# Optimization experiments

Measured on AMD Instinct MI355X. Metric: run time of the kernel, lower is better.

## Reference

```python
import jax, jax.numpy as jnp
import numpy as np

NUM_BINS = 8
TAIL_BOUND = 3.0
MIN_V = 1e-3
MIN_DERIV = 1e-3


def _normalize(u):
    # softmax -> min-width floor -> cumsum -> pad left -> map to [-tail, tail]
    v = jax.nn.softmax(u, axis=-1)
    v = MIN_V + (1.0 - MIN_V * NUM_BINS) * v
    cum = jnp.cumsum(v, axis=-1)
    cum = jnp.pad(cum, [(0, 0)] * (cum.ndim - 1) + [(1, 0)])
    return (cum - 0.5) * 2.0 * TAIL_BOUND, v


def _rqs(x_dyn, u_w, u_h, u_d):
    # x_dyn: [B, D]; u_w/u_h: [B, D, K]; u_d: [B, D, K+1]
    cum_w, w = _normalize(u_w)
    cum_h, h = _normalize(u_h)
    d = jax.nn.softplus(u_d) + MIN_DERIV
    cum_w = cum_w.at[..., -1].add(1e-6)  # searchsorted eps on last edge

    idx = jnp.sum((x_dyn[..., None] >= cum_w).astype(jnp.int32), axis=-1) - 1
    idx = jnp.clip(idx, 0, NUM_BINS - 1)[..., None]  # [B, D, 1]

    take = lambda a, i: jnp.take_along_axis(a, i, axis=-1)[..., 0]
    cw, ww = take(cum_w, idx), take(w, idx)
    ch, hh = take(cum_h, idx), take(h, idx)
    di = jnp.clip(take(d, idx), MIN_DERIV, 1000.0)
    di1 = jnp.clip(take(d, idx + 1), MIN_DERIV, 1000.0)

    delta = hh / ww
    theta = jnp.clip((x_dyn - cw) / ww, 0.0, 1.0)
    t1m = theta * (1.0 - theta)
    num_term = di1 * theta ** 2 + delta * t1m
    den = jnp.maximum(delta + (di + di1 - 2.0 * delta) * t1m, 1e-6)
    spline_out = ch + delta * num_term / den * ww
    deriv_num = delta ** 2 * (di1 * theta ** 2 + 2.0 * delta * t1m + di * (1.0 - theta) ** 2)
    spline_logdet = jnp.log(jnp.maximum(deriv_num / den ** 2, 1e-12))

    in_range = (x_dyn >= -TAIL_BOUND) & (x_dyn <= TAIL_BOUND)
    out = jnp.where(in_range, spline_out, x_dyn)
    logdet = jnp.where(in_range, spline_logdet, 0.0)
    return out, logdet


def setup_inputs() -> dict:
    key = jax.random.key(0)
    ks = jax.random.split(key, 3)
    B, D, H = 32768, 128, 256
    total = 3 * NUM_BINS + 1
    x = jax.random.normal(ks[0], (B, D), dtype=jnp.float32)
    mask = (jnp.arange(D) % 2).astype(jnp.float32)
    W1 = jax.random.normal(ks[1], (D, H), dtype=jnp.float32) * (1.0 / np.sqrt(D))
    b1 = jnp.zeros((H,), dtype=jnp.float32)
    W2 = jax.random.normal(ks[2], (H, D * total), dtype=jnp.float32) * (1.0 / np.sqrt(H))
    b2 = jnp.zeros((D * total,), dtype=jnp.float32)
    return {"x": x, "mask": mask, "W1": W1, "b1": b1, "W2": W2, "b2": b2}


def reference(x, mask, W1, b1, W2, b2):
    B, D = x.shape
    total = 3 * NUM_BINS + 1
    x_static = x * mask
    x_dyn = x * (1.0 - mask)
    hidden = jax.nn.relu(x_static @ W1 + b1)
    params = (hidden @ W2 + b2).reshape(B, D, total)
    u_w = params[..., :NUM_BINS]
    u_h = params[..., NUM_BINS:2 * NUM_BINS]
    u_d = params[..., 2 * NUM_BINS:]
    new_dyn, logdet = _rqs(x_dyn, u_w, u_h, u_d)
    out = x_static + new_dyn * (1.0 - mask)
    log_det = jnp.sum(logdet * (1.0 - mask), axis=1)
    return out, log_det
```

## Files before the change

### kernel.cpp

```cpp
#include <hip/hip_runtime.h>
#include <hip/hip_bf16.h>
#include <stdint.h>


#define B_ROWS 32768
#define DDIM   128
#define HDIM   256
#define NPACK  1664
#define LOSCALE 2048.0f
#define INV_LOSCALE (1.0f / 2048.0f)

using f32x4 = __attribute__((ext_vector_type(4))) float;
using f16x8 = __attribute__((ext_vector_type(8))) _Float16;
using f16x4 = __attribute__((ext_vector_type(4))) _Float16;

__device__ __forceinline__ void gl_lds16(const void* g, void* l) {
    __builtin_amdgcn_global_load_lds(
        (__attribute__((address_space(1))) void*)(void*)g,
        (__attribute__((address_space(3))) void*)l, 16, 0, 0);
}

__device__ __forceinline__ float rcpf(float x) { return __builtin_amdgcn_rcpf(x); }

__device__ __forceinline__ float softplus_fast(float z) {
    return fmaxf(z, 0.0f) + __logf(1.0f + __expf(-fabsf(z)));
}

__device__ __forceinline__ void rqs(const float* P, float xv, float& o, float& l) {
    float ew[8], vw[8], edw[9];
    float mw = P[0];
    #pragma unroll
    for (int j = 1; j < 8; ++j) mw = fmaxf(mw, P[j]);
    float sw = 0.0f;
    #pragma unroll
    for (int j = 0; j < 8; ++j) { ew[j] = expf(P[j] - mw); sw += ew[j]; }
    float rsw = rcpf(sw);
    float cum = 0.0f;
    edw[0] = -3.0f;
    #pragma unroll
    for (int j = 0; j < 8; ++j) {
        vw[j] = 0.001f + 0.992f * (ew[j] * rsw);
        cum += vw[j];
        edw[j + 1] = (cum - 0.5f) * 6.0f;
    }
    edw[8] += 1e-6f;

    float eh[8], vh[8], edh[9];
    float mh = P[8];
    #pragma unroll
    for (int j = 1; j < 8; ++j) mh = fmaxf(mh, P[8 + j]);
    float sh = 0.0f;
    #pragma unroll
    for (int j = 0; j < 8; ++j) { eh[j] = expf(P[8 + j] - mh); sh += eh[j]; }
    float rsh = rcpf(sh);
    float cumh = 0.0f;
    edh[0] = -3.0f;
    #pragma unroll
    for (int j = 0; j < 8; ++j) {
        vh[j] = 0.001f + 0.992f * (eh[j] * rsh);
        cumh += vh[j];
        edh[j + 1] = (cumh - 0.5f) * 6.0f;
    }

    float dk[9];
    #pragma unroll
    for (int j = 0; j < 9; ++j) dk[j] = softplus_fast(P[16 + j]) + 0.001f;

    int idx = -1;
    #pragma unroll
    for (int j = 0; j < 9; ++j) idx += (xv >= edw[j]) ? 1 : 0;
    idx = min(max(idx, 0), 7);

    float cw = edw[0], ww = vw[0], ch = edh[0], hh = vh[0], di = dk[0], di1 = dk[1];
    #pragma unroll
    for (int j = 0; j < 8; ++j) {
        bool sel = (idx == j);
        cw  = sel ? edw[j]    : cw;
        ww  = sel ? vw[j]     : ww;
        ch  = sel ? edh[j]    : ch;
        hh  = sel ? vh[j]     : hh;
        di  = sel ? dk[j]     : di;
        di1 = sel ? dk[j + 1] : di1;
    }
    di  = fminf(fmaxf(di,  0.001f), 1000.0f);
    di1 = fminf(fmaxf(di1, 0.001f), 1000.0f);

    float rww   = rcpf(ww);
    float delta = hh * rww;
    float theta = fminf(fmaxf((xv - cw) * rww, 0.0f), 1.0f);
    float t1m   = theta * (1.0f - theta);
    float th2   = theta * theta;
    float omt   = 1.0f - theta;
    float num_term = di1 * th2 + delta * t1m;
    float den      = fmaxf(delta + (di + di1 - 2.0f * delta) * t1m, 1e-6f);
    float rden     = rcpf(den);
    float sp       = ch + delta * num_term * rden * ww;
    float dn       = (delta * delta) * (di1 * th2 + 2.0f * delta * t1m + di * (omt * omt));
    float ld       = __logf(fmaxf(dn * rden * rden, 1e-12f));

    bool inr = (xv >= -3.0f) && (xv <= 3.0f);
    o = inr ? sp : xv;
    l = inr ? ld : 0.0f;
}

__global__ __launch_bounds__(256, 4) void k1_hidden(const float* __restrict__ x,
                                                    const float* __restrict__ W1,
                                                    const float* __restrict__ b1,
                                                    _Float16* __restrict__ hid_hi,
                                                    _Float16* __restrict__ hid_lo,
                                                    float* __restrict__ out,
                                                    float* __restrict__ logdet) {
    __shared__ float xodT[64][36];
    const int t  = threadIdx.x;
    const int rb = blockIdx.x * 32;
    const int cg = t & 63;
    const int rg = t >> 6;
    #pragma unroll
    for (int u = 0; u < 8; ++u) {
        int idx = u * 256 + t;
        int r = idx >> 6, k = idx & 63;
        float2 v = *(const float2*)&x[(rb + r) * DDIM + 2 * k];
        xodT[k][r] = v.y;
        *(float2*)&out[(rb + r) * DDIM + 2 * k] = v;
    }
    if (t < 32) logdet[rb + t] = 0.0f;
    __syncthreads();

    float acc[8][4];
    #pragma unroll
    for (int r = 0; r < 8; ++r)
        #pragma unroll
        for (int c = 0; c < 4; ++c) acc[r][c] = 0.0f;

    #pragma unroll 4
    for (int k = 0; k < 64; ++k) {
        float4 w  = *(const float4*)&W1[(2 * k + 1) * HDIM + cg * 4];
        float4 xa = *(const float4*)&xodT[k][rg * 8];
        float4 xb = *(const float4*)&xodT[k][rg * 8 + 4];
        float xr[8] = {xa.x, xa.y, xa.z, xa.w, xb.x, xb.y, xb.z, xb.w};
        float wc[4] = {w.x, w.y, w.z, w.w};
        #pragma unroll
        for (int r = 0; r < 8; ++r)
            #pragma unroll
            for (int c = 0; c < 4; ++c) acc[r][c] += xr[r] * wc[c];
    }

    float4 bias = *(const float4*)&b1[cg * 4];
    float bc[4] = {bias.x, bias.y, bias.z, bias.w};
    #pragma unroll
    for (int r = 0; r < 8; ++r) {
        int row = rb + rg * 8 + r;
        f16x4 vh, vl;
        #pragma unroll
        for (int c = 0; c < 4; ++c) {
            float h = fmaxf(acc[r][c] + bc[c], 0.0f);
            _Float16 hi = (_Float16)h;
            vh[c] = hi;
            vl[c] = (_Float16)((h - (float)hi) * LOSCALE);
        }
        *(f16x4*)&hid_hi[(size_t)row * HDIM + cg * 4] = vh;
        *(f16x4*)&hid_lo[(size_t)row * HDIM + cg * 4] = vl;
    }
}

__global__ __launch_bounds__(256) void k3_w2split(const float* __restrict__ W2,
                                                  _Float16* __restrict__ w2t_hi,
                                                  _Float16* __restrict__ w2t_lo) {
    int tid = blockIdx.x * 256 + threadIdx.x;
    int c  = tid >> 5;
    int kc = tid & 31;
    int bx = c >> 7;
    int cb = c & 127;
    int de = bx * 5 + cb / 25;
    int j  = cb % 25;
    bool valid = (cb < 125) && (de < 64);
    f16x8 vh, vl;
    #pragma unroll
    for (int i = 0; i < 8; ++i) {
        float v = valid ? W2[(size_t)(kc * 8 + i) * 3200 + 50 * de + j] : 0.0f;
        _Float16 h = (_Float16)v;
        vh[i] = h;
        vl[i] = (_Float16)((v - (float)h) * LOSCALE);
    }
    *(f16x8*)&w2t_hi[(size_t)c * HDIM + kc * 8] = vh;
    *(f16x8*)&w2t_lo[(size_t)c * HDIM + kc * 8] = vl;
}

__global__ __launch_bounds__(256, 2) void k2_mfma(
        const float* __restrict__ x,
        const _Float16* __restrict__ hid_hi, const _Float16* __restrict__ hid_lo,
        const _Float16* __restrict__ w2t_hi, const _Float16* __restrict__ w2t_lo,
        const float* __restrict__ b2,
        float* __restrict__ out, float* __restrict__ logdet) {
    __shared__ __align__(16) char smem[128 * 133 * 4];
    const int t    = threadIdx.x;
    const int lane = t & 63;
    const int wave = t >> 6;
    const int m0   = (wave & 1) * 64;
    const int n0   = (wave >> 1) * 64;
    const int row0 = blockIdx.y * 128;
    const int col0 = blockIdx.x * 128;

    f32x4 acc[4][4], acc2[4][4];
    #pragma unroll
    for (int i = 0; i < 4; ++i)
        #pragma unroll
        for (int j = 0; j < 4; ++j) {
            acc[i][j]  = (f32x4){0.f, 0.f, 0.f, 0.f};
            acc2[i][j] = (f32x4){0.f, 0.f, 0.f, 0.f};
        }

    for (int ks = 0; ks < 4; ++ks) {
        __syncthreads();
        #pragma unroll
        for (int call = 0; call < 4; ++call) {
            int g = call * 4 + wave;
            int s = g * 64 + lane;
            int r = s >> 3;
            int c = (s & 7) ^ (r & 7);
            int ke = ks * 64 + c * 8;
            char* ldsb = smem + g * 1024;
            gl_lds16(hid_hi + (size_t)(row0 + r) * HDIM + ke, ldsb);
            gl_lds16(hid_lo + (size_t)(row0 + r) * HDIM + ke, ldsb + 16384);
            gl_lds16(w2t_hi + (size_t)(col0 + r) * HDIM + ke, ldsb + 32768);
            gl_lds16(w2t_lo + (size_t)(col0 + r) * HDIM + ke, ldsb + 49152);
        }
        __syncthreads();
        #pragma unroll
        for (int kk = 0; kk < 2; ++kk) {
            int kc = kk * 4 + (lane >> 4);
            int sw = ((kc ^ (lane & 7)) << 4);
            f16x8 ah[4], al[4], bh[4], bl[4];
            #pragma unroll
            for (int i = 0; i < 4; ++i) {
                int oa = (m0 + i * 16 + (lane & 15)) * 128 + sw;
                ah[i] = *(const f16x8*)(smem + oa);
                al[i] = *(const f16x8*)(smem + 16384 + oa);
                int ob = (n0 + i * 16 + (lane & 15)) * 128 + sw;
                bh[i] = *(const f16x8*)(smem + 32768 + ob);
                bl[i] = *(const f16x8*)(smem + 49152 + ob);
            }
            #pragma unroll
            for (int mi = 0; mi < 4; ++mi)
                #pragma unroll
                for (int ni = 0; ni < 4; ++ni) {
                    acc[mi][ni]  = __builtin_amdgcn_mfma_f32_16x16x32_f16(ah[mi], bh[ni], acc[mi][ni],  0, 0, 0);
                    acc2[mi][ni] = __builtin_amdgcn_mfma_f32_16x16x32_f16(al[mi], bh[ni], acc2[mi][ni], 0, 0, 0);
                    acc2[mi][ni] = __builtin_amdgcn_mfma_f32_16x16x32_f16(ah[mi], bl[ni], acc2[mi][ni], 0, 0, 0);
                }
        }
    }

    __syncthreads();
    float* pf = (float*)smem;
    #pragma unroll
    for (int mi = 0; mi < 4; ++mi)
        #pragma unroll
        for (int ni = 0; ni < 4; ++ni)
            #pragma unroll
            for (int e = 0; e < 4; ++e) {
                int rl = m0 + mi * 16 + (lane >> 4) * 4 + e;
                int cl = n0 + ni * 16 + (lane & 15);
                pf[rl * 133 + cl] = acc[mi][ni][e] + acc2[mi][ni][e] * INV_LOSCALE;
            }
    __syncthreads();

    const int rl   = t & 127;
    const int rowg = blockIdx.y * 128 + rl;
    float ldsum = 0.0f;
    #pragma unroll
    for (int pass = 0; pass < 3; ++pass) {
        int dl = 2 * pass + (t >> 7);
        int de = blockIdx.x * 5 + dl;
        if (dl < 5 && de < 64) {
            float xv = x[(size_t)rowg * DDIM + 2 * de];
            float P[25];
            #pragma unroll
            for (int j = 0; j < 25; ++j)
                P[j] = pf[rl * 133 + dl * 25 + j] + b2[50 * de + j];
            float o, l;
            rqs(P, xv, o, l);
            out[(size_t)rowg * DDIM + 2 * de] = o;
            ldsum += l;
        }
    }
    atomicAdd(&logdet[rowg], ldsum);
}

extern "C" void kernel_launch(void* const* d_in, const int* in_sizes, int n_in,
                              void* d_out, int out_size, void* d_ws, size_t ws_size,
                              hipStream_t stream) {
    const float* x  = (const float*)d_in[0];
    const float* W1 = (const float*)d_in[2];
    const float* b1 = (const float*)d_in[3];
    const float* W2 = (const float*)d_in[4];
    const float* b2 = (const float*)d_in[5];

    float* out    = (float*)d_out;
    float* logdet = (float*)d_out + (size_t)B_ROWS * DDIM;

    _Float16* hid_hi = (_Float16*)d_ws;
    _Float16* hid_lo = hid_hi + (size_t)B_ROWS * HDIM;
    _Float16* w2t_hi = hid_lo + (size_t)B_ROWS * HDIM;
    _Float16* w2t_lo = w2t_hi + (size_t)NPACK * HDIM;

    k3_w2split<<<dim3(NPACK * 32 / 256), dim3(256), 0, stream>>>(W2, w2t_hi, w2t_lo);
    k1_hidden <<<dim3(B_ROWS / 32),      dim3(256), 0, stream>>>(x, W1, b1, hid_hi, hid_lo, out, logdet);
    k2_mfma   <<<dim3(NPACK / 128, B_ROWS / 128), dim3(256), 0, stream>>>(
        x, hid_hi, hid_lo, w2t_hi, w2t_lo, b2, out, logdet);
}
```

Before: 205.2 us.

## Double-buffer k2 LDS tiles and remap workgroups for XCD locality

The k2 GEMM main loop now runs over eight K-steps of 32 and double-buffers LDS: it issues global-to-LDS loads for the next step before computing the current one, with one barrier per step instead of two. The hi and lo halves are interleaved inside each buffer. Workgroup IDs in both k1 and k2 are remapped so that consecutive tiles land on the same XCD (wg&7 striding), which is meant to improve L2 reuse of shared hidden rows and W2 columns. The LDS footprint per buffer stays within the existing 68KB allocation, and the extra in-flight loads may raise register pressure.

```diff
diff --git a/kernel.cpp b/kernel.cpp
--- a/kernel.cpp
+++ b/kernel.cpp
@@ -112,7 +112,9 @@
                                                     float* __restrict__ logdet) {
     __shared__ float xodT[64][36];
     const int t  = threadIdx.x;
-    const int rb = blockIdx.x * 32;
+    const int wg = blockIdx.x;
+    const int lb = (wg & 7) * 128 + (wg >> 3);
+    const int rb = lb * 32;
     const int cg = t & 63;
     const int rg = t >> 6;
     #pragma unroll
@@ -198,8 +200,13 @@
     const int wave = t >> 6;
     const int m0   = (wave & 1) * 64;
     const int n0   = (wave >> 1) * 64;
-    const int row0 = blockIdx.y * 128;
-    const int col0 = blockIdx.x * 128;
+
+    const int wg = blockIdx.y * 13 + blockIdx.x;
+    const int lb = (wg & 7) * 416 + (wg >> 3);
+    const int bx = lb % 13;
+    const int by = lb / 13;
+    const int row0 = by * 128;
+    const int col0 = bx * 128;
 
     f32x4 acc[4][4], acc2[4][4];
     #pragma unroll
@@ -210,48 +217,56 @@
             acc2[i][j] = (f32x4){0.f, 0.f, 0.f, 0.f};
         }
 
-    for (int ks = 0; ks < 4; ++ks) {
+    auto stage = [&](int p, int ksx) {
+        #pragma unroll
+        for (int cc = 0; cc < 8; ++cc) {
+            int g  = cc * 4 + wave;
+            int gg = g & 15;
+            int rt = gg * 8 + (lane >> 3);
+            int c  = (lane & 7) ^ (rt & 7);
+            int ke = ksx * 32 + (c & 3) * 8;
+            char* ldsb = smem + p * 32768 + ((g >> 4) << 14) + gg * 1024;
+            if (g < 16) {
+                const _Float16* src = ((c < 4) ? hid_hi : hid_lo)
+                                      + (size_t)(row0 + rt) * HDIM + ke;
+                gl_lds16(src, ldsb);
+            } else {
+                const _Float16* src = ((c < 4) ? w2t_hi : w2t_lo)
+                                      + (size_t)(col0 + rt) * HDIM + ke;
+                gl_lds16(src, ldsb);
+            }
+        }
+    };
+
+    stage(0, 0);
+    __syncthreads();
+    int cur = 0;
+    for (int ks = 0; ks < 8; ++ks) {
+        if (ks < 7) stage(cur ^ 1, ks + 1);
+        const char* base = smem + cur * 32768;
+        const int kc = lane >> 4;
+        f16x8 ah[4], al[4], bh[4], bl[4];
+        #pragma unroll
+        for (int i = 0; i < 4; ++i) {
+            int ra = m0 + i * 16 + (lane & 15);
+            ah[i] = *(const f16x8*)(base + ra * 128 + ((kc ^ (ra & 7)) << 4));
+            al[i] = *(const f16x8*)(base + ra * 128 + (((kc | 4) ^ (ra & 7)) << 4));
+            int rb_ = n0 + i * 16 + (lane & 15);
+            bh[i] = *(const f16x8*)(base + 16384 + rb_ * 128 + ((kc ^ (rb_ & 7)) << 4));
+            bl[i] = *(const f16x8*)(base + 16384 + rb_ * 128 + (((kc | 4) ^ (rb_ & 7)) << 4));
+        }
+        #pragma unroll
+        for (int mi = 0; mi < 4; ++mi)
+            #pragma unroll
+            for (int ni = 0; ni < 4; ++ni) {
+                acc[mi][ni]  = __builtin_amdgcn_mfma_f32_16x16x32_f16(ah[mi], bh[ni], acc[mi][ni],  0, 0, 0);
+                acc2[mi][ni] = __builtin_amdgcn_mfma_f32_16x16x32_f16(al[mi], bh[ni], acc2[mi][ni], 0, 0, 0);
+                acc2[mi][ni] = __builtin_amdgcn_mfma_f32_16x16x32_f16(ah[mi], bl[ni], acc2[mi][ni], 0, 0, 0);
+            }
         __syncthreads();
-        #pragma unroll
-        for (int call = 0; call < 4; ++call) {
-            int g = call * 4 + wave;
-            int s = g * 64 + lane;
-            int r = s >> 3;
-            int c = (s & 7) ^ (r & 7);
-            int ke = ks * 64 + c * 8;
-            char* ldsb = smem + g * 1024;
-            gl_lds16(hid_hi + (size_t)(row0 + r) * HDIM + ke, ldsb);
-            gl_lds16(hid_lo + (size_t)(row0 + r) * HDIM + ke, ldsb + 16384);
-            gl_lds16(w2t_hi + (size_t)(col0 + r) * HDIM + ke, ldsb + 32768);
-            gl_lds16(w2t_lo + (size_t)(col0 + r) * HDIM + ke, ldsb + 49152);
-        }
-        __syncthreads();
-        #pragma unroll
-        for (int kk = 0; kk < 2; ++kk) {
-            int kc = kk * 4 + (lane >> 4);
-            int sw = ((kc ^ (lane & 7)) << 4);
-            f16x8 ah[4], al[4], bh[4], bl[4];
-            #pragma unroll
-            for (int i = 0; i < 4; ++i) {
-                int oa = (m0 + i * 16 + (lane & 15)) * 128 + sw;
-                ah[i] = *(const f16x8*)(smem + oa);
-                al[i] = *(const f16x8*)(smem + 16384 + oa);
-                int ob = (n0 + i * 16 + (lane & 15)) * 128 + sw;
-                bh[i] = *(const f16x8*)(smem + 32768 + ob);
-                bl[i] = *(const f16x8*)(smem + 49152 + ob);
-            }
-            #pragma unroll
-            for (int mi = 0; mi < 4; ++mi)
-                #pragma unroll
-                for (int ni = 0; ni < 4; ++ni) {
-                    acc[mi][ni]  = __builtin_amdgcn_mfma_f32_16x16x32_f16(ah[mi], bh[ni], acc[mi][ni],  0, 0, 0);
-                    acc2[mi][ni] = __builtin_amdgcn_mfma_f32_16x16x32_f16(al[mi], bh[ni], acc2[mi][ni], 0, 0, 0);
-                    acc2[mi][ni] = __builtin_amdgcn_mfma_f32_16x16x32_f16(ah[mi], bl[ni], acc2[mi][ni], 0, 0, 0);
-                }
-        }
-    }
-
-    __syncthreads();
+        cur ^= 1;
+    }
+
     float* pf = (float*)smem;
     #pragma unroll
     for (int mi = 0; mi < 4; ++mi)
@@ -266,12 +281,12 @@
     __syncthreads();
 
     const int rl   = t & 127;
-    const int rowg = blockIdx.y * 128 + rl;
+    const int rowg = row0 + rl;
     float ldsum = 0.0f;
     #pragma unroll
     for (int pass = 0; pass < 3; ++pass) {
         int dl = 2 * pass + (t >> 7);
-        int de = blockIdx.x * 5 + dl;
+        int de = bx * 5 + dl;
         if (dl < 5 && de < 64) {
             float xv = x[(size_t)rowg * DDIM + 2 * de];
             float P[25];
@@ -306,6 +321,6 @@
 
     k3_w2split<<<dim3(NPACK * 32 / 256), dim3(256), 0, stream>>>(W2, w2t_hi, w2t_lo);
     k1_hidden <<<dim3(B_ROWS / 32),      dim3(256), 0, stream>>>(x, W1, b1, hid_hi, hid_lo, out, logdet);
-    k2_mfma   <<<dim3(NPACK / 128, B_ROWS / 128), dim3(256), 0, stream>>>(
+    k2_mfma   <<<dim3(13, B_ROWS / 128), dim3(256), 0, stream>>>(
         x, hid_hi, hid_lo, w2t_hi, w2t_lo, b2, out, logdet);
 }
```

After: 330.9 us. +61.2%, slower.
